# Kernel tuning notes

Hardware: AMD Instinct MI355X
Metric: run time of the kernel (lower is better)

The kernel has to match this reference:

```python
import jax, jax.numpy as jnp
from jax import lax
import numpy as np

NX = 512
LENGTH = 0.1
BCS = [[[0.025, 0.0], [0.075, 0.0]]]
BATCH = 32
COF = 0.25 * (LENGTH / (NX - 1)) ** 2  # 0.25 * stride^2 / temper_coefficient


def _make_mask():
    # Dirichlet boundary mask G (1 in interior, 0 on bc segments), per torch logic
    G = np.ones((1, 1, NX, NX), dtype=np.float32)
    for bc in BCS:
        if bc[0][1] == 0 and bc[1][1] == 0:
            i0 = round(bc[0][0] * NX / LENGTH); i1 = round(bc[1][0] * NX / LENGTH)
            G[..., i0:i1, :1] = 0.0
        elif bc[0][1] == LENGTH and bc[1][1] == LENGTH:
            i0 = round(bc[0][0] * NX / LENGTH); i1 = round(bc[1][0] * NX / LENGTH)
            G[..., i0:i1, -1:] = 0.0
        elif bc[0][0] == 0 and bc[1][0] == 0:
            i0 = round(bc[0][1] * NX / LENGTH); i1 = round(bc[1][1] * NX / LENGTH)
            G[..., :1, i0:i1] = 0.0
        elif bc[0][0] == LENGTH and bc[1][0] == LENGTH:
            i0 = round(bc[0][1] * NX / LENGTH); i1 = round(bc[1][1] * NX / LENGTH)
            G[..., -1:, i0:i1] = 0.0
        else:
            raise ValueError('bc error!')
    return jnp.asarray(G)

G_MASK = _make_mask()


def setup_inputs() -> dict:
    key = jax.random.key(0)
    k1, k2 = jax.random.split(key)
    layout = jax.random.normal(k1, (BATCH, 1, NX, NX), dtype=jnp.float32)
    heat = jax.random.normal(k2, (BATCH, 1, NX, NX), dtype=jnp.float32)
    return {"layout": layout, "heat": heat, "n_iter": 20}


def reference(layout, heat, n_iter):
    f = COF * layout  # source term
    G = G_MASK

    def step(x, _):
        # reflect-pad then 5-point (cross) stencil average == conv2d with the
        # [[0,.25,0],[.25,0,.25],[0,.25,0]] kernel
        p = jnp.pad(x, ((0, 0), (0, 0), (1, 1), (1, 1)), mode='reflect')
        jac = 0.25 * (p[..., :-2, 1:-1] + p[..., 2:, 1:-1]
                      + p[..., 1:-1, :-2] + p[..., 1:-1, 2:])
        return G * (jac + f), None

    # first torch iteration pads heat*G; subsequent iterations pad x (already masked)
    x, _ = lax.scan(step, heat * G, None, length=n_iter)
    return x
```

## Files before the change

### kernel.cpp

```cpp
#include <hip/hip_runtime.h>


constexpr int NXc   = 512;
constexpr int QC    = 128;
constexpr int BATCHc= 32;
constexpr int K     = 5;
constexpr int R     = 16;
constexpr int VMAX  = R + 2 * K;
constexpr int HALF  = VMAX / 2;
constexpr int NBANDS= (NXc / R) * BATCHc;
constexpr int GRID  = NBANDS / 2;
constexpr int MR0   = 128;
constexpr int MR1   = 384;

template <bool FIRST>
__global__ __launch_bounds__(256)
void jacobi_fused(const float* __restrict__ src, const float* __restrict__ layout,
                  float* __restrict__ dst, float cof)
{
    __shared__ float4 lds4[VMAX * QC];
    float* ldsf = reinterpret_cast<float*>(lds4);

    const int tid   = threadIdx.x;
    const int c4    = tid & (QC - 1);
    const int h     = tid >> 7;
    const int vbase = h * HALF;

    for (int band = blockIdx.x; band < NBANDS; band += GRID) {
        const int bi  = band >> 5;
        const int br  = band & 31;
        const int r0  = br * R;
        const bool top = (r0 == 0), bot = (r0 + R == NXc);
        const int H0  = top ? 0 : K;
        const int V   = H0 + R + (bot ? 0 : K);
        const int v0g = r0 - H0;
        const size_t base = (size_t)bi * NXc * QC;
        const float4* __restrict__ srcq = reinterpret_cast<const float4*>(src) + base;
        const float4* __restrict__ layq = reinterpret_cast<const float4*>(layout) + base;
        float4* __restrict__ dstq = reinterpret_cast<float4*>(dst) + base;

        __syncthreads();

        float4 fr[HALF];
        #pragma unroll
        for (int j = 0; j < HALF; ++j) {
            const int v  = vbase + j;
            const int gc = (v < V) ? (v0g + v) : v0g;
            float4 val = srcq[(size_t)gc * QC + c4];
            if (FIRST) {
                if (c4 == 0 && gc >= MR0 && gc < MR1) val.x = 0.f;
            }
            if (v < V) lds4[v * QC + c4] = val;
            const float4 f = layq[(size_t)gc * QC + c4];
            fr[j] = make_float4(cof * f.x, cof * f.y, cof * f.z, cof * f.w);
        }
        __syncthreads();

        for (int t = 1; t <= K; ++t) {
            const int a = top ? 0 : t;
            const int b = V - (bot ? 0 : t);

            float4 res[HALF];
            float4 up_r = lds4[((vbase > 0) ? vbase - 1 : 0) * QC + c4];
            float4 cur  = lds4[vbase * QC + c4];
            #pragma unroll
            for (int j = 0; j < HALF; ++j) {
                const int v  = vbase + j;
                const int g  = v0g + v;
                const int vn = (v + 1 < V) ? v + 1 : V - 1;
                const int vr = (v < V) ? v : V - 1;
                const float4 nxt = lds4[vn * QC + c4];
                const float4 upe = (g == 0)       ? nxt  : up_r;
                const float4 dne = (g == NXc - 1) ? up_r : nxt;
                const float lf = (c4 == 0)      ? cur.y : ldsf[vr * NXc + (c4 << 2) - 1];
                const float rt = (c4 == QC - 1) ? cur.z : ldsf[vr * NXc + (c4 << 2) + 4];
                float4 o;
                o.x = 0.25f * (((upe.x + dne.x) + lf   ) + cur.y) + fr[j].x;
                o.y = 0.25f * (((upe.y + dne.y) + cur.x) + cur.z) + fr[j].y;
                o.z = 0.25f * (((upe.z + dne.z) + cur.y) + cur.w) + fr[j].z;
                o.w = 0.25f * (((upe.w + dne.w) + cur.z) + rt   ) + fr[j].w;
                if (c4 == 0 && g >= MR0 && g < MR1) o.x = 0.f;
                res[j] = o;
                up_r = cur; cur = nxt;
            }
            __syncthreads();
            #pragma unroll
            for (int j = 0; j < HALF; ++j) {
                const int v = vbase + j;
                if (v >= a && v < b) lds4[v * QC + c4] = res[j];
            }
            __syncthreads();
        }

        #pragma unroll
        for (int j = 0; j < HALF; ++j) {
            const int v = vbase + j;
            if (v >= H0 && v < H0 + R) {
                const int g = v0g + v;
                dstq[(size_t)g * QC + c4] = lds4[v * QC + c4];
            }
        }
    }
}

extern "C" void kernel_launch(void* const* d_in, const int* in_sizes, int n_in,
                              void* d_out, int out_size, void* d_ws, size_t ws_size,
                              hipStream_t stream)
{
    const float* layout = (const float*)d_in[0];
    const float* heat   = (const float*)d_in[1];
    float* out = (float*)d_out;
    float* ws  = (float*)d_ws;

    const float cof = (float)(0.25 * (0.1 / 511.0) * (0.1 / 511.0));

    dim3 grid(GRID), block(256);
    jacobi_fused<true ><<<grid, block, 0, stream>>>(heat, layout, ws,  cof);
    jacobi_fused<false><<<grid, block, 0, stream>>>(ws,   layout, out, cof);
    jacobi_fused<false><<<grid, block, 0, stream>>>(out,  layout, ws,  cof);
    jacobi_fused<false><<<grid, block, 0, stream>>>(ws,   layout, out, cof);
}
```

Measured before the change: 163.5 us.

## Use 512-thread blocks, shallower temporal tiling, and wavefront shuffles for horizontal neighbours

Each fused launch now advances 4 iterations instead of 5, so the kernel runs five times instead of four. The halo shrinks from 5 to 4 rows per side, which cuts redundant halo loads and compute per band. Each block handles one band with 512 threads in four row groups instead of looping over two bands with 256 threads. Left and right horizontal neighbours now come from __shfl_up/__shfl_down within the 64-lane wavefront, with LDS reads only at wavefront edges, replacing two scalar LDS reads per point. The cost is one extra launch plus one more full global read and write of the field.

```diff
diff --git a/kernel.cpp b/kernel.cpp
--- a/kernel.cpp
+++ b/kernel.cpp
@@ -1,104 +1,107 @@
 #include <hip/hip_runtime.h>
 
 
-constexpr int NXc   = 512;
-constexpr int QC    = 128;
-constexpr int BATCHc= 32;
-constexpr int K     = 5;
-constexpr int R     = 16;
-constexpr int VMAX  = R + 2 * K;
-constexpr int HALF  = VMAX / 2;
-constexpr int NBANDS= (NXc / R) * BATCHc;
-constexpr int GRID  = NBANDS / 2;
-constexpr int MR0   = 128;
-constexpr int MR1   = 384;
+constexpr int NXc    = 512;
+constexpr int QC     = 128;
+constexpr int K      = 4;
+constexpr int R      = 16;
+constexpr int VMAX   = R + 2 * K;
+constexpr int GROUPS = 4;
+constexpr int HALF   = VMAX / GROUPS;
+constexpr int NBANDS = (NXc / R) * 32;
+constexpr int MR0    = 128;
+constexpr int MR1    = 384;
 
 template <bool FIRST>
-__global__ __launch_bounds__(256)
+__global__ __launch_bounds__(512, 6)
 void jacobi_fused(const float* __restrict__ src, const float* __restrict__ layout,
                   float* __restrict__ dst, float cof)
 {
     __shared__ float4 lds4[VMAX * QC];
     float* ldsf = reinterpret_cast<float*>(lds4);
 
-    const int tid   = threadIdx.x;
-    const int c4    = tid & (QC - 1);
-    const int h     = tid >> 7;
-    const int vbase = h * HALF;
+    const int tid    = threadIdx.x;
+    const int c4     = tid & (QC - 1);
+    const int grp    = tid >> 7;
+    const int vstart = grp * HALF;
+    const int lane   = tid & 63;
 
-    for (int band = blockIdx.x; band < NBANDS; band += GRID) {
-        const int bi  = band >> 5;
-        const int br  = band & 31;
-        const int r0  = br * R;
-        const bool top = (r0 == 0), bot = (r0 + R == NXc);
-        const int H0  = top ? 0 : K;
-        const int V   = H0 + R + (bot ? 0 : K);
-        const int v0g = r0 - H0;
-        const size_t base = (size_t)bi * NXc * QC;
-        const float4* __restrict__ srcq = reinterpret_cast<const float4*>(src) + base;
-        const float4* __restrict__ layq = reinterpret_cast<const float4*>(layout) + base;
-        float4* __restrict__ dstq = reinterpret_cast<float4*>(dst) + base;
+    const int band = blockIdx.x;
+    const int bi   = band >> 5;
+    const int br   = band & 31;
+    const int r0   = br * R;
+    const bool top = (r0 == 0), bot = (r0 + R == NXc);
+    const int H0   = top ? 0 : K;
+    const int V    = H0 + R + (bot ? 0 : K);
+    const int v0g  = r0 - H0;
+    const size_t base = (size_t)bi * NXc * QC;
+    const float4* __restrict__ srcq = reinterpret_cast<const float4*>(src) + base;
+    const float4* __restrict__ layq = reinterpret_cast<const float4*>(layout) + base;
+    float4* __restrict__ dstq = reinterpret_cast<float4*>(dst) + base;
 
-        __syncthreads();
+    float4 fr[HALF];
+    #pragma unroll
+    for (int j = 0; j < HALF; ++j) {
+        const int v  = vstart + j;
+        const int gc = (v < V) ? (v0g + v) : (v0g + V - 1);
+        float4 val = srcq[(size_t)gc * QC + c4];
+        if (FIRST) {
+            if (c4 == 0 && gc >= MR0 && gc < MR1) val.x = 0.f;
+        }
+        if (v < V) lds4[v * QC + c4] = val;
+        const float4 f = layq[(size_t)gc * QC + c4];
+        fr[j] = make_float4(cof * f.x, cof * f.y, cof * f.z, cof * f.w);
+    }
+    __syncthreads();
 
-        float4 fr[HALF];
+    #pragma unroll
+    for (int t = 1; t <= K; ++t) {
+        const int a = top ? 0 : t;
+        const int b = V - (bot ? 0 : t);
+
+        float4 res[HALF];
+        float4 up_r = lds4[((vstart > 0) ? vstart - 1 : 0) * QC + c4];
+        float4 cur  = lds4[vstart * QC + c4];
         #pragma unroll
         for (int j = 0; j < HALF; ++j) {
-            const int v  = vbase + j;
-            const int gc = (v < V) ? (v0g + v) : v0g;
-            float4 val = srcq[(size_t)gc * QC + c4];
-            if (FIRST) {
-                if (c4 == 0 && gc >= MR0 && gc < MR1) val.x = 0.f;
-            }
-            if (v < V) lds4[v * QC + c4] = val;
-            const float4 f = layq[(size_t)gc * QC + c4];
-            fr[j] = make_float4(cof * f.x, cof * f.y, cof * f.z, cof * f.w);
+            const int v  = vstart + j;
+            const int g  = v0g + v;
+            const int vr = (v < V) ? v : V - 1;
+            const int vn = (v + 1 < V) ? v + 1 : V - 1;
+            const float4 nxt = lds4[vn * QC + c4];
+            const float4 upe = (g == 0)       ? nxt  : up_r;
+            const float4 dne = (g == NXc - 1) ? up_r : nxt;
+
+            float lf = __shfl_up(cur.w, 1);
+            float rt = __shfl_down(cur.x, 1);
+            if (c4 == 0)           lf = cur.y;
+            else if (lane == 0)    lf = ldsf[vr * NXc + (c4 << 2) - 1];
+            if (c4 == QC - 1)      rt = cur.z;
+            else if (lane == 63)   rt = ldsf[vr * NXc + (c4 << 2) + 4];
+
+            float4 o;
+            o.x = 0.25f * (((upe.x + dne.x) + lf   ) + cur.y) + fr[j].x;
+            o.y = 0.25f * (((upe.y + dne.y) + cur.x) + cur.z) + fr[j].y;
+            o.z = 0.25f * (((upe.z + dne.z) + cur.y) + cur.w) + fr[j].z;
+            o.w = 0.25f * (((upe.w + dne.w) + cur.z) + rt   ) + fr[j].w;
+            if (c4 == 0 && g >= MR0 && g < MR1) o.x = 0.f;
+            res[j] = o;
+            up_r = cur; cur = nxt;
         }
         __syncthreads();
-
-        for (int t = 1; t <= K; ++t) {
-            const int a = top ? 0 : t;
-            const int b = V - (bot ? 0 : t);
-
-            float4 res[HALF];
-            float4 up_r = lds4[((vbase > 0) ? vbase - 1 : 0) * QC + c4];
-            float4 cur  = lds4[vbase * QC + c4];
-            #pragma unroll
-            for (int j = 0; j < HALF; ++j) {
-                const int v  = vbase + j;
-                const int g  = v0g + v;
-                const int vn = (v + 1 < V) ? v + 1 : V - 1;
-                const int vr = (v < V) ? v : V - 1;
-                const float4 nxt = lds4[vn * QC + c4];
-                const float4 upe = (g == 0)       ? nxt  : up_r;
-                const float4 dne = (g == NXc - 1) ? up_r : nxt;
-                const float lf = (c4 == 0)      ? cur.y : ldsf[vr * NXc + (c4 << 2) - 1];
-                const float rt = (c4 == QC - 1) ? cur.z : ldsf[vr * NXc + (c4 << 2) + 4];
-                float4 o;
-                o.x = 0.25f * (((upe.x + dne.x) + lf   ) + cur.y) + fr[j].x;
-                o.y = 0.25f * (((upe.y + dne.y) + cur.x) + cur.z) + fr[j].y;
-                o.z = 0.25f * (((upe.z + dne.z) + cur.y) + cur.w) + fr[j].z;
-                o.w = 0.25f * (((upe.w + dne.w) + cur.z) + rt   ) + fr[j].w;
-                if (c4 == 0 && g >= MR0 && g < MR1) o.x = 0.f;
-                res[j] = o;
-                up_r = cur; cur = nxt;
-            }
-            __syncthreads();
-            #pragma unroll
-            for (int j = 0; j < HALF; ++j) {
-                const int v = vbase + j;
-                if (v >= a && v < b) lds4[v * QC + c4] = res[j];
-            }
-            __syncthreads();
-        }
-
         #pragma unroll
         for (int j = 0; j < HALF; ++j) {
-            const int v = vbase + j;
-            if (v >= H0 && v < H0 + R) {
-                const int g = v0g + v;
-                dstq[(size_t)g * QC + c4] = lds4[v * QC + c4];
-            }
+            const int v = vstart + j;
+            if (v >= a && v < b) lds4[v * QC + c4] = res[j];
+        }
+        __syncthreads();
+    }
+
+    #pragma unroll
+    for (int j = 0; j < HALF; ++j) {
+        const int v = vstart + j;
+        if (v >= H0 && v < H0 + R) {
+            dstq[(size_t)(v0g + v) * QC + c4] = lds4[v * QC + c4];
         }
     }
 }
@@ -114,8 +117,9 @@
 
     const float cof = (float)(0.25 * (0.1 / 511.0) * (0.1 / 511.0));
 
-    dim3 grid(GRID), block(256);
-    jacobi_fused<true ><<<grid, block, 0, stream>>>(heat, layout, ws,  cof);
+    dim3 grid(NBANDS), block(512);
+    jacobi_fused<true ><<<grid, block, 0, stream>>>(heat, layout, out, cof);
+    jacobi_fused<false><<<grid, block, 0, stream>>>(out,  layout, ws,  cof);
     jacobi_fused<false><<<grid, block, 0, stream>>>(ws,   layout, out, cof);
     jacobi_fused<false><<<grid, block, 0, stream>>>(out,  layout, ws,  cof);
     jacobi_fused<false><<<grid, block, 0, stream>>>(ws,   layout, out, cof);
```

Result: slower. 461.3 us (+182.1%).
